# Kernel tuning notes

Measured on AMD Instinct MI355X. Metric: run time of the kernel, lower is better.

The kernel has to match this reference:

```python
import jax, jax.numpy as jnp
import numpy as np

EPS = 1e-5

def _bn(x, g, b):
    # training-mode BatchNorm3d over (N, T, H, W) per channel (axis=1), biased variance
    red = (0, 2, 3, 4)
    m = x.mean(red, keepdims=True)
    v = x.var(red, keepdims=True)
    s = (1, -1, 1, 1, 1)
    return (x - m) / jnp.sqrt(v + EPS) * g.reshape(s) + b.reshape(s)

def _conv3d(x, w, b):
    # Conv3d kernel (1,3,3), padding (0,1,1)
    y = jax.lax.conv_general_dilated(x, w, (1, 1, 1), ((0, 0), (1, 1), (1, 1)),
                                     dimension_numbers=('NCDHW', 'OIDHW', 'NCDHW'))
    return y + b[None, :, None, None, None]

def _forward(x1, x2, attn_weight, W_up, b_up, W_mlp, b_mlp, g_mlp, be_mlp,
             W_c1, b_c1, g_c1, be_c1, W_c2, b_c2, g_c2, be_c2):
    w2 = W_up[:, :, 0]  # [Cin, Cout, 2, 2]
    y = jnp.einsum('bcthw,cokl->bothkwl', x1, w2)
    b_, o, t, h, k, w_, l = y.shape
    x1u = y.reshape(b_, o, t, h * k, w_ * l) + b_up[None, :, None, None, None]

    bs, d_in, T, H, W = x2.shape
    nH = attn_weight.shape[0]
    hh, ww = attn_weight.shape[2], attn_weight.shape[3]
    # [nH, bs, h, w, T, T] -> [nH*bs, T*T, h, w], bilinear upsample to (H, W)
    A = attn_weight.transpose(0, 1, 4, 5, 2, 3).reshape(nH * bs, T * T, hh, ww)
    A = jax.image.resize(A, (nH * bs, T * T, H, W), method='linear')
    A = A.reshape(nH, bs, T, T, H, W)
    # per-(head,b,H,W) temporal attention matmul: avoids materializing x2.repeat(n_head,...)
    ctx = jnp.einsum('nbtsxy,bcsxy->btxycn', A, x2)  # [bs,T,H,W,d_in,nH]
    ctx = ctx.reshape(bs, T, H, W, d_in * nH)        # flatten order (c, n) matches torch permute+view
    hmlp = jnp.einsum('btxyk,ko->btxyo', ctx, W_mlp) + b_mlp
    hmlp = hmlp.transpose(0, 4, 1, 2, 3)  # [bs, enc, T, H, W]
    hmlp = jax.nn.relu(_bn(hmlp, g_mlp, be_mlp))

    x = jnp.concatenate([hmlp, x1u], axis=1)  # [bs, enc+dec, T, H, W]
    x = jax.nn.relu(_bn(_conv3d(x, W_c1, b_c1), g_c1, be_c1))
    x = jax.nn.relu(_bn(_conv3d(x, W_c2, b_c2), g_c2, be_c2))
    return x

def setup_inputs() -> dict:
    key = jax.random.key(0)
    ks = jax.random.split(key, 8)
    bs, T, H, W = 2, 8, 128, 128
    dec, enc, nH = 64, 32, 4
    hh = ww = 16  # attn_scale_factor = 8
    return {
        'x1': jax.random.normal(ks[0], (bs, dec, T, H // 2, W // 2), jnp.float32),
        'x2': jax.random.normal(ks[1], (bs, enc, T, H, W), jnp.float32),
        'attn_weight': jax.random.uniform(ks[2], (nH, bs, hh, ww, T, T), jnp.float32),
        'W_up': jax.random.normal(ks[3], (dec, dec, 1, 2, 2), jnp.float32) * 0.05,
        'b_up': jnp.zeros((dec,), jnp.float32),
        'W_mlp': jax.random.normal(ks[4], (nH * enc, enc), jnp.float32) * 0.05,
        'b_mlp': jnp.zeros((enc,), jnp.float32),
        'g_mlp': jnp.ones((enc,), jnp.float32),
        'be_mlp': jnp.zeros((enc,), jnp.float32),
        'W_c1': jax.random.normal(ks[5], (enc, dec + enc, 1, 3, 3), jnp.float32) * 0.05,
        'b_c1': jnp.zeros((enc,), jnp.float32),
        'g_c1': jnp.ones((enc,), jnp.float32),
        'be_c1': jnp.zeros((enc,), jnp.float32),
        'W_c2': jax.random.normal(ks[6], (enc, enc, 1, 3, 3), jnp.float32) * 0.05,
        'b_c2': jnp.zeros((enc,), jnp.float32),
        'g_c2': jnp.ones((enc,), jnp.float32),
        'be_c2': jnp.zeros((enc,), jnp.float32),
    }

def reference(x1, x2, attn_weight, W_up, b_up, W_mlp, b_mlp, g_mlp, be_mlp,
              W_c1, b_c1, g_c1, be_c1, W_c2, b_c2, g_c2, be_c2):
    return _forward(x1, x2, attn_weight, W_up, b_up, W_mlp, b_mlp, g_mlp, be_mlp,
                    W_c1, b_c1, g_c1, be_c1, W_c2, b_c2, g_c2, be_c2)
```

## Files before the change

kernel.cpp:

```cpp
#include <hip/hip_runtime.h>


#define EPSV 1e-5f

typedef __attribute__((ext_vector_type(8))) short short8;
typedef __attribute__((ext_vector_type(4))) short short4v;
typedef __attribute__((ext_vector_type(4))) float floatx4;

__device__ inline short f2bf(float f) {
  union { float f; unsigned u; } v; v.f = f;
  unsigned r = (v.u + 0x7fffu + ((v.u >> 16) & 1u)) >> 16;
  return (short)r;
}
__device__ inline float bf2f(short s) {
  union { unsigned u; float f; } v; v.u = ((unsigned)(unsigned short)s) << 16;
  return v.f;
}

#define UB_OFF   0
#define HMB_OFF  8388608
#define C1B_OFF  12582912
#define C2B_OFF  16777216
#define X2T_OFF  20971520
#define WB1_OFF  29360128
#define WB2_OFF  29373952
#define WUP_OFF  29378560
#define WMB_OFF  29386752
#define ST_OFF   29388800
#define SC_OFF   29388992

__global__ __launch_bounds__(256) void k_repackb(const float* __restrict__ Wc1, const float* __restrict__ Wc2,
        const float* __restrict__ Wup, const float* __restrict__ Wmlp,
        short* __restrict__ wb1, short* __restrict__ wb2, short* __restrict__ wupb, short* __restrict__ wmb) {
  int i = blockIdx.x*256 + threadIdx.x;
  if (i < 27648) {
    int cc = i / 9216, r = i % 9216;
    int tap = r / 1024, r2 = r % 1024;
    int nt = r2 >> 9, lane = (r2 >> 3) & 63, j = r2 & 7;
    int o = nt*16 + (lane & 15);
    int cin = cc*32 + (lane >> 4)*8 + j;
    wb1[i] = f2bf(Wc1[(o*96 + cin)*9 + tap]);
  }
  if (i < 9216) {
    int tap = i / 1024, r2 = i % 1024;
    int nt = r2 >> 9, lane = (r2 >> 3) & 63, j = r2 & 7;
    int o = nt*16 + (lane & 15);
    int cin = (lane >> 4)*8 + j;
    wb2[i] = f2bf(Wc2[(o*32 + cin)*9 + tap]);
  }
  if (i < 16384) {
    int j = i & 7, lane = (i >> 3) & 63, r = i >> 9;
    int nt = r & 3, kb = (r >> 2) & 1, p = r >> 3;
    int c = kb*32 + (lane >> 4)*8 + j;
    int o = nt*16 + (lane & 15);
    wupb[i] = f2bf(Wup[(c*64 + o)*4 + p]);
  }
  if (i < 4096) {
    int j = i & 7, lane = (i >> 3) & 63, nt = (i >> 9) & 1, ck = i >> 10;
    int k = ck*32 + (lane >> 4)*8 + j;
    int o = nt*16 + (lane & 15);
    wmb[i] = f2bf(Wmlp[k*32 + o]);
  }
}

__global__ __launch_bounds__(256) void k_x2t(const float* __restrict__ x2, short* __restrict__ x2t) {
  __shared__ short lds[32*264];
  int s = blockIdx.y, b = blockIdx.z;
  int tile = blockIdx.x;
  int tid = threadIdx.x;
  #pragma unroll
  for (int k=0; k<8; ++k) {
    int f4 = k*256 + tid;
    int c = f4 >> 6, p4 = f4 & 63;
    float4 v = *(const float4*)(x2 + ((long)(b*32+c)*8 + s)*16384 + tile*256 + p4*4);
    short4v o;
    o[0]=f2bf(v.x); o[1]=f2bf(v.y); o[2]=f2bf(v.z); o[3]=f2bf(v.w);
    *(short4v*)(lds + c*264 + p4*4) = o;
  }
  __syncthreads();
  short* dst = x2t + (((long)(b*8+s)*16384) + tile*256 + tid)*32;
  #pragma unroll
  for (int g=0; g<4; ++g) {
    short8 v;
    #pragma unroll
    for (int j=0; j<8; ++j) v[j] = lds[(g*8+j)*264 + tid];
    *(short8*)(dst + g*8) = v;
  }
}

__global__ __launch_bounds__(256) void k_up_mfma(const float* __restrict__ x1,
        const short* __restrict__ wupb, const float* __restrict__ bup,
        short* __restrict__ Ub) {
  __shared__ __align__(16) char smem[34816];
  short8* stage = (short8*)smem;
  int t = blockIdx.y, b = blockIdx.z;
  int chunk = blockIdx.x >> 2, parity = blockIdx.x & 3;
  int tid = threadIdx.x, lane = tid & 63, w = tid >> 6;

  {
    const float* xp = x1 + ((long)(b*64)*8 + t)*4096 + chunk*256 + tid;
    #pragma unroll
    for (int o8 = 0; o8 < 8; ++o8) {
      short8 v;
      #pragma unroll
      for (int j = 0; j < 8; ++j) v[j] = f2bf(xp[(long)(o8*8+j)*32768]);
      int kb = o8 >> 2, cq = o8 & 3;
      stage[(kb*16 + (tid>>4))*64 + cq*16 + (tid&15)] = v;
    }
  }
  __syncthreads();

  floatx4 acc[4][4];
  #pragma unroll
  for (int nt=0; nt<4; ++nt) {
    float bb = bup[nt*16 + (lane&15)];
    #pragma unroll
    for (int mt=0; mt<4; ++mt) acc[mt][nt] = (floatx4){bb,bb,bb,bb};
  }
  const short8* wp = (const short8*)wupb;
  #pragma unroll
  for (int kb=0; kb<2; ++kb) {
    short8 bfr[4];
    #pragma unroll
    for (int nt=0; nt<4; ++nt) bfr[nt] = wp[((parity*2+kb)*4+nt)*64 + lane];
    #pragma unroll
    for (int mt=0; mt<4; ++mt) {
      short8 a = stage[(kb*16 + w*4 + mt)*64 + lane];
      #pragma unroll
      for (int nt=0; nt<4; ++nt)
        acc[mt][nt] = __builtin_amdgcn_mfma_f32_16x16x32_bf16(a, bfr[nt], acc[mt][nt], 0,0,0);
    }
  }

  __syncthreads();
  short* trb = (short*)smem;
  #pragma unroll
  for (int mt=0; mt<4; ++mt)
    #pragma unroll
    for (int nt=0; nt<4; ++nt)
      #pragma unroll
      for (int r=0; r<4; ++r)
        trb[(w*64 + mt*16 + (lane>>4)*4 + r)*68 + nt*16 + (lane&15)] = f2bf(acc[mt][nt][r]);
  __syncthreads();

  int ip = chunk*256 + tid;
  int X = 2*(ip>>6) + (parity>>1), Y = 2*(ip&63) + (parity&1);
  short* dst = Ub + (((long)(b*8+t)*16384 + X*128 + Y)*64);
  const short* src = trb + tid*68;
  #pragma unroll
  for (int k=0; k<16; ++k)
    *(short4v*)(dst + k*4) = *(const short4v*)(src + k*4);
}

__global__ __launch_bounds__(256) void k_ctxmlp(const short* __restrict__ x2t,
        const float* __restrict__ attn, const short* __restrict__ wmb,
        const float* __restrict__ bmlp, short* __restrict__ HMb, float* __restrict__ st) {
  __shared__ float la[2048];
  __shared__ __align__(16) short ctxs[256*40];
  __shared__ float sb[64];
  int t = blockIdx.y, b = blockIdx.z;
  int tid = threadIdx.x, lane = tid & 63, w = tid >> 6;
  int m = lane & 15, kg = lane >> 4;
  int pos = blockIdx.x*256 + tid;
  if (tid < 64) sb[tid] = 0.f;

  int x0 = blockIdx.x*2;
  int ixbase = max((int)floorf((x0+0.5f)*0.125f - 0.5f), 0);

  float4* la4 = (float4*)la;
  const float4* g4 = (const float4*)attn;
  #pragma unroll
  for (int k=0;k<2;++k) {
    int f = k*256 + tid;
    int s4 = f & 1, iy = (f>>1)&15, slot = (f>>5)&3, n = f>>7;
    int ixs = min(ixbase + slot, 15);
    la4[f] = g4[((((n*2+b)*16+ixs)*16+iy)*8+t)*2 + s4];
  }
  __syncthreads();

  int x = pos >> 7, y = pos & 127;
  float ux = (x+0.5f)*0.125f - 0.5f;
  float uy = (y+0.5f)*0.125f - 0.5f;
  int ix0 = (int)floorf(ux), iy0 = (int)floorf(uy);
  float fx = ux - (float)ix0, fy = uy - (float)iy0;
  int sa  = max(ix0,0) - ixbase;
  int sbl = min(ix0+1,15) - ixbase;
  int iya = max(iy0,0), iyb = min(iy0+1,15);
  float w00=(1.f-fx)*(1.f-fy), w01=(1.f-fx)*fy, w10=fx*(1.f-fy), w11=fx*fy;
  float a[4][8];
  #pragma unroll
  for (int n=0;n<4;++n) {
    const float4* p00 = la4 + ((n*4+sa )*16+iya)*2;
    const float4* p01 = la4 + ((n*4+sa )*16+iyb)*2;
    const float4* p10 = la4 + ((n*4+sbl)*16+iya)*2;
    const float4* p11 = la4 + ((n*4+sbl)*16+iyb)*2;
    #pragma unroll
    for (int q=0;q<2;++q) {
      float4 c00=p00[q], c01=p01[q], c10=p10[q], c11=p11[q];
      a[n][q*4+0] = w00*c00.x + w01*c01.x + w10*c10.x + w11*c11.x;
      a[n][q*4+1] = w00*c00.y + w01*c01.y + w10*c10.y + w11*c11.y;
      a[n][q*4+2] = w00*c00.z + w01*c01.z + w10*c10.z + w11*c11.z;
      a[n][q*4+3] = w00*c00.w + w01*c01.w + w10*c10.w + w11*c11.w;
    }
  }

  float b0v = bmlp[m], b1v = bmlp[16+m];
  floatx4 acc[4][2];
  #pragma unroll
  for (int mt=0; mt<4; ++mt) {
    acc[mt][0] = (floatx4){b0v,b0v,b0v,b0v};
    acc[mt][1] = (floatx4){b1v,b1v,b1v,b1v};
  }

  const short8* wm = (const short8*)wmb;
  for (int ck=0; ck<4; ++ck) {
    short8 xr[8];
    #pragma unroll
    for (int s=0;s<8;++s)
      xr[s] = *(const short8*)(x2t + (((long)(b*8+s)*16384) + pos)*32 + ck*8);
    float ctx[8][4];
    #pragma unroll
    for (int c=0;c<8;++c) { ctx[c][0]=0.f; ctx[c][1]=0.f; ctx[c][2]=0.f; ctx[c][3]=0.f; }
    #pragma unroll
    for (int s=0;s<8;++s) {
      float xv[8];
      #pragma unroll
      for (int c=0;c<8;++c) xv[c] = bf2f(xr[s][c]);
      #pragma unroll
      for (int n=0;n<4;++n) {
        float an = a[n][s];
        #pragma unroll
        for (int c=0;c<8;++c) ctx[c][n] = fmaf(an, xv[c], ctx[c][n]);
      }
    }
    #pragma unroll
    for (int g=0; g<4; ++g) {
      short8 v;
      #pragma unroll
      for (int j=0;j<8;++j) { int kl = g*8+j; v[j] = f2bf(ctx[kl>>2][kl&3]); }
      *(short8*)(ctxs + tid*40 + g*8) = v;
    }
    __syncthreads();
    short8 wb0 = wm[(ck*2+0)*64 + lane];
    short8 wb1f = wm[(ck*2+1)*64 + lane];
    #pragma unroll
    for (int mt=0; mt<4; ++mt) {
      short8 af = *(const short8*)(ctxs + ((w*4+mt)*16 + m)*40 + kg*8);
      acc[mt][0] = __builtin_amdgcn_mfma_f32_16x16x32_bf16(af, wb0,  acc[mt][0], 0,0,0);
      acc[mt][1] = __builtin_amdgcn_mfma_f32_16x16x32_bf16(af, wb1f, acc[mt][1], 0,0,0);
    }
    __syncthreads();
  }

  float s0=0.f,q0=0.f,s1=0.f,q1=0.f;
  #pragma unroll
  for (int mt=0; mt<4; ++mt)
    #pragma unroll
    for (int r=0; r<4; ++r) {
      float v0 = acc[mt][0][r]; s0 += v0; q0 += v0*v0;
      float v1 = acc[mt][1][r]; s1 += v1; q1 += v1*v1;
    }
  s0 += __shfl_xor(s0,16); s0 += __shfl_xor(s0,32);
  q0 += __shfl_xor(q0,16); q0 += __shfl_xor(q0,32);
  s1 += __shfl_xor(s1,16); s1 += __shfl_xor(s1,32);
  q1 += __shfl_xor(q1,16); q1 += __shfl_xor(q1,32);
  if (lane < 16) {
    atomicAdd(&sb[lane],    s0); atomicAdd(&sb[16+lane], s1);
    atomicAdd(&sb[32+lane], q0); atomicAdd(&sb[48+lane], q1);
  }

  short* tr = ctxs;
  #pragma unroll
  for (int mt=0; mt<4; ++mt) {
    int tile = w*4 + mt;
    #pragma unroll
    for (int nt=0; nt<2; ++nt)
      #pragma unroll
      for (int r=0; r<4; ++r)
        tr[(tile*16 + kg*4 + r)*32 + nt*16 + m] = f2bf(acc[mt][nt][r]);
  }
  __syncthreads();
  long slab = (long)(b*8+t)*16384;
  short8* d8 = (short8*)(HMb + (slab + blockIdx.x*256 + tid)*32);
  const short8* s8 = (const short8*)(tr + tid*32);
  d8[0]=s8[0]; d8[1]=s8[1]; d8[2]=s8[2]; d8[3]=s8[3];
  if (tid < 64) atomicAdd(&st[tid], sb[tid]);
}

__global__ void k_finalize(const float* __restrict__ st, const float* __restrict__ g,
                           const float* __restrict__ be, float* __restrict__ sc, float* __restrict__ sh) {
  int c = threadIdx.x;
  if (c < 32) {
    float mean = st[c] * (1.f/262144.f);
    float var  = st[32+c] * (1.f/262144.f) - mean*mean;
    float s = g[c] / sqrtf(var + EPSV);
    sc[c] = s;
    sh[c] = be[c] - mean*s;
  }
}

template<int NCHUNK>
__global__ __launch_bounds__(256) void k_convp(
    const short* __restrict__ src0, const short* __restrict__ srcU,
    const short* __restrict__ wb, const float* __restrict__ bias,
    const float* __restrict__ sc, const float* __restrict__ sh,
    short* __restrict__ dstCL, float* __restrict__ st) {
  constexpr int NBUF = (NCHUNK > 1) ? 2 : 1;
  __shared__ __align__(16) short stage[NBUF][324*40];
  __shared__ float sbuf[64];
  int t = blockIdx.y, b = blockIdx.z;
  int tid = threadIdx.x, lane = tid & 63, w = tid >> 6;
  if (tid < 64) sbuf[tid] = 0.f;
  long slab = (long)(b*8+t)*16384;
  int x0 = (int)(blockIdx.x >> 3) * 16, y0 = (int)(blockIdx.x & 7) * 16;
  int m = lane & 15, kg = lane >> 4;

  int pA = tid;        int rA = pA/18, cA = pA - rA*18;
  int XA = x0-1+rA, YA = y0-1+cA;
  bool okA = ((unsigned)XA < 128u) & ((unsigned)YA < 128u);
  int pB = tid + 256;  bool hasB = pB < 324;
  int rB = pB/18, cB = pB - rB*18;
  int XB = x0-1+rB, YB = y0-1+cB;
  bool okB = hasB && (((unsigned)XB < 128u) & ((unsigned)YB < 128u));
  long offA = slab + XA*128 + YA, offB = slab + XB*128 + YB;

  short8 preA[4], preB[4];

  float bias0 = bias[m], bias1 = bias[16 + m];
  floatx4 acc[4][2];
  #pragma unroll
  for (int mt=0; mt<4; ++mt) {
    acc[mt][0] = (floatx4){bias0,bias0,bias0,bias0};
    acc[mt][1] = (floatx4){bias1,bias1,bias1,bias1};
  }

  {
    const short* sA = src0 + offA*32;
    const short* sB = src0 + offB*32;
    #pragma unroll
    for (int g=0; g<4; ++g) {
      preA[g] = okA ? *(const short8*)(sA + g*8) : (short8)0;
      preB[g] = okB ? *(const short8*)(sB + g*8) : (short8)0;
    }
  }
  #pragma unroll
  for (int g=0; g<4; ++g) {
    short8 vA, vB;
    #pragma unroll
    for (int j=0;j<8;++j) {
      int ch = g*8+j;
      float scv = sc[ch], shv = sh[ch];
      vA[j] = okA ? f2bf(fmaxf(fmaf(bf2f(preA[g][j]), scv, shv), 0.f)) : (short)0;
      vB[j] = okB ? f2bf(fmaxf(fmaf(bf2f(preB[g][j]), scv, shv), 0.f)) : (short)0;
    }
    *(short8*)(&stage[0][pA*40 + g*8]) = vA;
    if (hasB) *(short8*)(&stage[0][pB*40 + g*8]) = vB;
  }
  __syncthreads();

  const short8* wbp = (const short8*)wb;
  #pragma unroll
  for (int cc=0; cc<NCHUNK; ++cc) {
    if (cc+1 < NCHUNK) {
      int coff = cc*32;
      const short* sA = srcU + offA*64 + coff;
      const short* sB = srcU + offB*64 + coff;
      #pragma unroll
      for (int g=0; g<4; ++g) {
        preA[g] = okA ? *(const short8*)(sA + g*8) : (short8)0;
        preB[g] = okB ? *(const short8*)(sB + g*8) : (short8)0;
      }
    }
    #pragma unroll
    for (int tap=0; tap<9; ++tap) {
      int dy = tap/3, dx = tap - 3*dy;
      short8 b0 = wbp[((cc*9+tap)*2+0)*64 + lane];
      short8 b1 = wbp[((cc*9+tap)*2+1)*64 + lane];
      #pragma unroll
      for (int mt=0; mt<4; ++mt) {
        int p = (w*4 + mt + dy)*18 + m + dx;
        short8 a = *(const short8*)(&stage[cc & (NBUF-1)][p*40 + kg*8]);
        acc[mt][0] = __builtin_amdgcn_mfma_f32_16x16x32_bf16(a, b0, acc[mt][0], 0,0,0);
        acc[mt][1] = __builtin_amdgcn_mfma_f32_16x16x32_bf16(a, b1, acc[mt][1], 0,0,0);
      }
    }
    if (cc+1 < NCHUNK) {
      #pragma unroll
      for (int g=0; g<4; ++g) {
        *(short8*)(&stage[(cc+1) & (NBUF-1)][pA*40 + g*8]) = preA[g];
        if (hasB) *(short8*)(&stage[(cc+1) & (NBUF-1)][pB*40 + g*8]) = preB[g];
      }
    }
    __syncthreads();
  }

  float s0=0.f,q0=0.f,s1=0.f,q1=0.f;
  #pragma unroll
  for (int mt=0; mt<4; ++mt)
    #pragma unroll
    for (int r=0; r<4; ++r) {
      float v0 = acc[mt][0][r]; s0 += v0; q0 += v0*v0;
      float v1 = acc[mt][1][r]; s1 += v1; q1 += v1*v1;
    }
  s0 += __shfl_xor(s0,16); s0 += __shfl_xor(s0,32);
  q0 += __shfl_xor(q0,16); q0 += __shfl_xor(q0,32);
  s1 += __shfl_xor(s1,16); s1 += __shfl_xor(s1,32);
  q1 += __shfl_xor(q1,16); q1 += __shfl_xor(q1,32);
  if (lane < 16) {
    atomicAdd(&sbuf[lane],    s0); atomicAdd(&sbuf[16+lane], s1);
    atomicAdd(&sbuf[32+lane], q0); atomicAdd(&sbuf[48+lane], q1);
  }

  short* tr = &stage[0][0];
  #pragma unroll
  for (int mt=0; mt<4; ++mt) {
    int tile = w*4 + mt;
    #pragma unroll
    for (int nt=0; nt<2; ++nt)
      #pragma unroll
      for (int r=0; r<4; ++r)
        tr[(tile*16 + kg*4 + r)*32 + nt*16 + m] = f2bf(acc[mt][nt][r]);
  }
  __syncthreads();
  int px = tid >> 4, py = tid & 15;
  short8* d8 = (short8*)(dstCL + ((slab + (long)(x0+px)*128 + (y0+py))*32));
  const short8* s8 = (const short8*)(tr + tid*32);
  d8[0]=s8[0]; d8[1]=s8[1]; d8[2]=s8[2]; d8[3]=s8[3];
  if (tid < 64) atomicAdd(&st[tid], sbuf[tid]);
}

__global__ __launch_bounds__(256) void k_bnrelu2(const short* __restrict__ C2b,
        const float* __restrict__ sc, const float* __restrict__ sh,
        float* __restrict__ out) {
  __shared__ float tb[10592];
  int t = blockIdx.y, b = blockIdx.z;
  int posbase = blockIdx.x * 256;
  int tid = threadIdx.x;
  long slab = (long)(b*8+t)*16384;
  {
    const short8* sp = (const short8*)(C2b + (slab + posbase + tid)*32);
    int pi = tid + (tid>>5)*8;
    #pragma unroll
    for (int g=0; g<4; ++g) {
      short8 v = sp[g];
      #pragma unroll
      for (int j=0; j<8; ++j) {
        int ch = g*8+j;
        tb[ch*321 + pi] = fmaxf(fmaf(bf2f(v[j]), sc[ch], sh[ch]), 0.f);
      }
    }
  }
  __syncthreads();
  int ch = tid >> 3, pg = tid & 7;
  float* op = out + ((long)(b*32+ch)*8 + t)*16384 + posbase + pg*32;
  const float* tp = tb + ch*321 + pg*40;
  #pragma unroll
  for (int k=0; k<8; ++k) {
    float4 v;
    v.x = tp[k*4+0]; v.y = tp[k*4+1]; v.z = tp[k*4+2]; v.w = tp[k*4+3];
    *(float4*)(op + k*4) = v;
  }
}

extern "C" void kernel_launch(void* const* d_in, const int* in_sizes, int n_in,
                              void* d_out, int out_size, void* d_ws, size_t ws_size,
                              hipStream_t stream) {
  (void)in_sizes; (void)n_in; (void)out_size; (void)ws_size;
  const float* x1   = (const float*)d_in[0];
  const float* x2   = (const float*)d_in[1];
  const float* attn = (const float*)d_in[2];
  const float* Wup  = (const float*)d_in[3];
  const float* bup  = (const float*)d_in[4];
  const float* Wmlp = (const float*)d_in[5];
  const float* bmlp = (const float*)d_in[6];
  const float* gmlp = (const float*)d_in[7];
  const float* bemlp= (const float*)d_in[8];
  const float* Wc1  = (const float*)d_in[9];
  const float* bc1  = (const float*)d_in[10];
  const float* gc1  = (const float*)d_in[11];
  const float* bec1 = (const float*)d_in[12];
  const float* Wc2  = (const float*)d_in[13];
  const float* bc2  = (const float*)d_in[14];
  const float* gc2  = (const float*)d_in[15];
  const float* bec2 = (const float*)d_in[16];
  float* ws  = (float*)d_ws;
  float* out = (float*)d_out;

  short* Ub   = (short*)(ws + UB_OFF);
  short* HMb  = (short*)(ws + HMB_OFF);
  short* C1b  = (short*)(ws + C1B_OFF);
  short* C2b  = (short*)(ws + C2B_OFF);
  short* x2t  = (short*)(ws + X2T_OFF);
  short* wb1  = (short*)(ws + WB1_OFF);
  short* wb2  = (short*)(ws + WB2_OFF);
  short* wupb = (short*)(ws + WUP_OFF);
  short* wmb  = (short*)(ws + WMB_OFF);
  float* st1  = ws + ST_OFF;
  float* st2  = st1 + 64;
  float* st3  = st2 + 64;
  float* sc1  = ws + SC_OFF;  float* sh1 = sc1+32;
  float* sc2  = sh1+32;       float* sh2 = sc2+32;
  float* sc3  = sh2+32;       float* sh3 = sc3+32;

  hipMemsetAsync(st1, 0, 192*sizeof(float), stream);
  k_repackb<<<108, 256, 0, stream>>>(Wc1, Wc2, Wup, Wmlp, wb1, wb2, wupb, wmb);
  k_x2t<<<dim3(64,8,2), 256, 0, stream>>>(x2, x2t);
  k_up_mfma<<<dim3(64,8,2), 256, 0, stream>>>(x1, wupb, bup, Ub);
  k_ctxmlp<<<dim3(64,8,2), 256, 0, stream>>>(x2t, attn, wmb, bmlp, HMb, st1);
  k_finalize<<<1, 32, 0, stream>>>(st1, gmlp, bemlp, sc1, sh1);
  k_convp<3><<<dim3(64,8,2), 256, 0, stream>>>(HMb, Ub, wb1, bc1, sc1, sh1, C1b, st2);
  k_finalize<<<1, 32, 0, stream>>>(st2, gc1, bec1, sc2, sh2);
  k_convp<1><<<dim3(64,8,2), 256, 0, stream>>>(C1b, nullptr, wb2, bc2, sc2, sh2, C2b, st3);
  k_finalize<<<1, 32, 0, stream>>>(st3, gc2, bec2, sc3, sh3);
  k_bnrelu2<<<dim3(64,8,2), 256, 0, stream>>>(C2b, sc3, sh3, out);
}
```

Measured before the change: 308.0 us.

## Drop x2 transpose and finalize kernels; fuse BN stat finalize into consumers

Removes the k_x2t pass so k_ctxmlp reads fp32 x2 directly in channel-first layout. This saves a full read-convert-write pass over x2 but gives up the bf16 vectorised loads. It also removes the three single-block k_finalize launches by computing BN scale and shift per block in shared memory inside the conv and bnrelu kernels. The conv kernel now uses a single stage buffer with an extra barrier between chunks, and hoists the weight fragments for all nine taps into registers before each chunk. That adds register pressure and a serialising sync in exchange for half the LDS.

```diff
diff --git a/kernel.cpp b/kernel.cpp
--- a/kernel.cpp
+++ b/kernel.cpp
@@ -21,13 +21,11 @@
 #define HMB_OFF  8388608
 #define C1B_OFF  12582912
 #define C2B_OFF  16777216
-#define X2T_OFF  20971520
-#define WB1_OFF  29360128
-#define WB2_OFF  29373952
-#define WUP_OFF  29378560
-#define WMB_OFF  29386752
-#define ST_OFF   29388800
-#define SC_OFF   29388992
+#define WB1_OFF  20971520
+#define WB2_OFF  20985344
+#define WUP_OFF  20989952
+#define WMB_OFF  20998144
+#define ST_OFF   21000192
 
 __global__ __launch_bounds__(256) void k_repackb(const float* __restrict__ Wc1, const float* __restrict__ Wc2,
         const float* __restrict__ Wup, const float* __restrict__ Wmlp,
@@ -63,40 +61,16 @@
   }
 }
 
-__global__ __launch_bounds__(256) void k_x2t(const float* __restrict__ x2, short* __restrict__ x2t) {
-  __shared__ short lds[32*264];
-  int s = blockIdx.y, b = blockIdx.z;
-  int tile = blockIdx.x;
-  int tid = threadIdx.x;
-  #pragma unroll
-  for (int k=0; k<8; ++k) {
-    int f4 = k*256 + tid;
-    int c = f4 >> 6, p4 = f4 & 63;
-    float4 v = *(const float4*)(x2 + ((long)(b*32+c)*8 + s)*16384 + tile*256 + p4*4);
-    short4v o;
-    o[0]=f2bf(v.x); o[1]=f2bf(v.y); o[2]=f2bf(v.z); o[3]=f2bf(v.w);
-    *(short4v*)(lds + c*264 + p4*4) = o;
-  }
-  __syncthreads();
-  short* dst = x2t + (((long)(b*8+s)*16384) + tile*256 + tid)*32;
-  #pragma unroll
-  for (int g=0; g<4; ++g) {
-    short8 v;
-    #pragma unroll
-    for (int j=0; j<8; ++j) v[j] = lds[(g*8+j)*264 + tid];
-    *(short8*)(dst + g*8) = v;
-  }
-}
-
-__global__ __launch_bounds__(256) void k_up_mfma(const float* __restrict__ x1,
+__global__ __launch_bounds__(256) void k_up(const float* __restrict__ x1,
         const short* __restrict__ wupb, const float* __restrict__ bup,
         short* __restrict__ Ub) {
   __shared__ __align__(16) char smem[34816];
+  int bid = blockIdx.x;
+  int tid = threadIdx.x;
+  int cp = bid & 63, t = (bid >> 6) & 7, b = bid >> 9;
+  int chunk = cp >> 2, parity = cp & 3;
+  int lane = tid & 63, w = tid >> 6;
   short8* stage = (short8*)smem;
-  int t = blockIdx.y, b = blockIdx.z;
-  int chunk = blockIdx.x >> 2, parity = blockIdx.x & 3;
-  int tid = threadIdx.x, lane = tid & 63, w = tid >> 6;
-
   {
     const float* xp = x1 + ((long)(b*64)*8 + t)*4096 + chunk*256 + tid;
     #pragma unroll
@@ -152,7 +126,7 @@
     *(short4v*)(dst + k*4) = *(const short4v*)(src + k*4);
 }
 
-__global__ __launch_bounds__(256) void k_ctxmlp(const short* __restrict__ x2t,
+__global__ __launch_bounds__(256) void k_ctxmlp(const float* __restrict__ x2,
         const float* __restrict__ attn, const short* __restrict__ wmb,
         const float* __restrict__ bmlp, short* __restrict__ HMb, float* __restrict__ st) {
   __shared__ float la[2048];
@@ -213,24 +187,21 @@
   }
 
   const short8* wm = (const short8*)wmb;
+  const float* x2p = x2 + (long)b*4194304 + pos;
   for (int ck=0; ck<4; ++ck) {
-    short8 xr[8];
-    #pragma unroll
-    for (int s=0;s<8;++s)
-      xr[s] = *(const short8*)(x2t + (((long)(b*8+s)*16384) + pos)*32 + ck*8);
     float ctx[8][4];
     #pragma unroll
     for (int c=0;c<8;++c) { ctx[c][0]=0.f; ctx[c][1]=0.f; ctx[c][2]=0.f; ctx[c][3]=0.f; }
     #pragma unroll
     for (int s=0;s<8;++s) {
-      float xv[8];
-      #pragma unroll
-      for (int c=0;c<8;++c) xv[c] = bf2f(xr[s][c]);
-      #pragma unroll
-      for (int n=0;n<4;++n) {
-        float an = a[n][s];
-        #pragma unroll
-        for (int c=0;c<8;++c) ctx[c][n] = fmaf(an, xv[c], ctx[c][n]);
+      float a0=a[0][s], a1=a[1][s], a2=a[2][s], a3=a[3][s];
+      #pragma unroll
+      for (int c=0;c<8;++c) {
+        float xv = x2p[(long)((ck*8+c)*8 + s)*16384];
+        ctx[c][0] = fmaf(a0, xv, ctx[c][0]);
+        ctx[c][1] = fmaf(a1, xv, ctx[c][1]);
+        ctx[c][2] = fmaf(a2, xv, ctx[c][2]);
+        ctx[c][3] = fmaf(a3, xv, ctx[c][3]);
       }
     }
     #pragma unroll
@@ -287,30 +258,26 @@
   if (tid < 64) atomicAdd(&st[tid], sb[tid]);
 }
 
-__global__ void k_finalize(const float* __restrict__ st, const float* __restrict__ g,
-                           const float* __restrict__ be, float* __restrict__ sc, float* __restrict__ sh) {
-  int c = threadIdx.x;
-  if (c < 32) {
-    float mean = st[c] * (1.f/262144.f);
-    float var  = st[32+c] * (1.f/262144.f) - mean*mean;
-    float s = g[c] / sqrtf(var + EPSV);
-    sc[c] = s;
-    sh[c] = be[c] - mean*s;
-  }
-}
-
 template<int NCHUNK>
 __global__ __launch_bounds__(256) void k_convp(
     const short* __restrict__ src0, const short* __restrict__ srcU,
     const short* __restrict__ wb, const float* __restrict__ bias,
-    const float* __restrict__ sc, const float* __restrict__ sh,
-    short* __restrict__ dstCL, float* __restrict__ st) {
-  constexpr int NBUF = (NCHUNK > 1) ? 2 : 1;
-  __shared__ __align__(16) short stage[NBUF][324*40];
+    const float* __restrict__ stIn, const float* __restrict__ gam,
+    const float* __restrict__ bet,
+    short* __restrict__ dstCL, float* __restrict__ stOut) {
+  __shared__ __align__(16) short stage[324*40];
   __shared__ float sbuf[64];
+  __shared__ float scs[32], shs[32];
   int t = blockIdx.y, b = blockIdx.z;
   int tid = threadIdx.x, lane = tid & 63, w = tid >> 6;
   if (tid < 64) sbuf[tid] = 0.f;
+  if (tid < 32) {
+    float mean = stIn[tid] * (1.f/262144.f);
+    float var  = stIn[32+tid] * (1.f/262144.f) - mean*mean;
+    float s = gam[tid] / sqrtf(var + EPSV);
+    scs[tid] = s;
+    shs[tid] = bet[tid] - mean*s;
+  }
   long slab = (long)(b*8+t)*16384;
   int x0 = (int)(blockIdx.x >> 3) * 16, y0 = (int)(blockIdx.x & 7) * 16;
   int m = lane & 15, kg = lane >> 4;
@@ -343,24 +310,31 @@
       preB[g] = okB ? *(const short8*)(sB + g*8) : (short8)0;
     }
   }
+  __syncthreads();
   #pragma unroll
   for (int g=0; g<4; ++g) {
     short8 vA, vB;
     #pragma unroll
     for (int j=0;j<8;++j) {
       int ch = g*8+j;
-      float scv = sc[ch], shv = sh[ch];
+      float scv = scs[ch], shv = shs[ch];
       vA[j] = okA ? f2bf(fmaxf(fmaf(bf2f(preA[g][j]), scv, shv), 0.f)) : (short)0;
       vB[j] = okB ? f2bf(fmaxf(fmaf(bf2f(preB[g][j]), scv, shv), 0.f)) : (short)0;
     }
-    *(short8*)(&stage[0][pA*40 + g*8]) = vA;
-    if (hasB) *(short8*)(&stage[0][pB*40 + g*8]) = vB;
+    *(short8*)(&stage[pA*40 + g*8]) = vA;
+    if (hasB) *(short8*)(&stage[pB*40 + g*8]) = vB;
   }
   __syncthreads();
 
   const short8* wbp = (const short8*)wb;
   #pragma unroll
   for (int cc=0; cc<NCHUNK; ++cc) {
+    short8 Bf0[9], Bf1[9];
+    #pragma unroll
+    for (int tap=0; tap<9; ++tap) {
+      Bf0[tap] = wbp[((cc*9+tap)*2+0)*64 + lane];
+      Bf1[tap] = wbp[((cc*9+tap)*2+1)*64 + lane];
+    }
     if (cc+1 < NCHUNK) {
       int coff = cc*32;
       const short* sA = srcU + offA*64 + coff;
@@ -374,24 +348,23 @@
     #pragma unroll
     for (int tap=0; tap<9; ++tap) {
       int dy = tap/3, dx = tap - 3*dy;
-      short8 b0 = wbp[((cc*9+tap)*2+0)*64 + lane];
-      short8 b1 = wbp[((cc*9+tap)*2+1)*64 + lane];
       #pragma unroll
       for (int mt=0; mt<4; ++mt) {
         int p = (w*4 + mt + dy)*18 + m + dx;
-        short8 a = *(const short8*)(&stage[cc & (NBUF-1)][p*40 + kg*8]);
-        acc[mt][0] = __builtin_amdgcn_mfma_f32_16x16x32_bf16(a, b0, acc[mt][0], 0,0,0);
-        acc[mt][1] = __builtin_amdgcn_mfma_f32_16x16x32_bf16(a, b1, acc[mt][1], 0,0,0);
+        short8 a = *(const short8*)(&stage[p*40 + kg*8]);
+        acc[mt][0] = __builtin_amdgcn_mfma_f32_16x16x32_bf16(a, Bf0[tap], acc[mt][0], 0,0,0);
+        acc[mt][1] = __builtin_amdgcn_mfma_f32_16x16x32_bf16(a, Bf1[tap], acc[mt][1], 0,0,0);
       }
     }
     if (cc+1 < NCHUNK) {
+      __syncthreads();
       #pragma unroll
       for (int g=0; g<4; ++g) {
-        *(short8*)(&stage[(cc+1) & (NBUF-1)][pA*40 + g*8]) = preA[g];
-        if (hasB) *(short8*)(&stage[(cc+1) & (NBUF-1)][pB*40 + g*8]) = preB[g];
+        *(short8*)(&stage[pA*40 + g*8]) = preA[g];
+        if (hasB) *(short8*)(&stage[pB*40 + g*8]) = preB[g];
       }
-    }
-    __syncthreads();
+      __syncthreads();
+    }
   }
 
   float s0=0.f,q0=0.f,s1=0.f,q1=0.f;
@@ -411,7 +384,8 @@
     atomicAdd(&sbuf[32+lane], q0); atomicAdd(&sbuf[48+lane], q1);
   }
 
-  short* tr = &stage[0][0];
+  __syncthreads();
+  short* tr = &stage[0];
   #pragma unroll
   for (int mt=0; mt<4; ++mt) {
     int tile = w*4 + mt;
@@ -426,27 +400,38 @@
   short8* d8 = (short8*)(dstCL + ((slab + (long)(x0+px)*128 + (y0+py))*32));
   const short8* s8 = (const short8*)(tr + tid*32);
   d8[0]=s8[0]; d8[1]=s8[1]; d8[2]=s8[2]; d8[3]=s8[3];
-  if (tid < 64) atomicAdd(&st[tid], sbuf[tid]);
+  if (tid < 64) atomicAdd(&stOut[tid], sbuf[tid]);
 }
 
 __global__ __launch_bounds__(256) void k_bnrelu2(const short* __restrict__ C2b,
-        const float* __restrict__ sc, const float* __restrict__ sh,
-        float* __restrict__ out) {
+        const float* __restrict__ stIn, const float* __restrict__ gam,
+        const float* __restrict__ bet, float* __restrict__ out) {
   __shared__ float tb[10592];
+  __shared__ float scs[32], shs[32];
   int t = blockIdx.y, b = blockIdx.z;
   int posbase = blockIdx.x * 256;
   int tid = threadIdx.x;
+  if (tid < 32) {
+    float mean = stIn[tid] * (1.f/262144.f);
+    float var  = stIn[32+tid] * (1.f/262144.f) - mean*mean;
+    float s = gam[tid] / sqrtf(var + EPSV);
+    scs[tid] = s;
+    shs[tid] = bet[tid] - mean*s;
+  }
   long slab = (long)(b*8+t)*16384;
+  const short8* sp = (const short8*)(C2b + (slab + posbase + tid)*32);
+  short8 v[4];
+  #pragma unroll
+  for (int g=0; g<4; ++g) v[g] = sp[g];
+  __syncthreads();
   {
-    const short8* sp = (const short8*)(C2b + (slab + posbase + tid)*32);
     int pi = tid + (tid>>5)*8;
     #pragma unroll
     for (int g=0; g<4; ++g) {
-      short8 v = sp[g];
       #pragma unroll
       for (int j=0; j<8; ++j) {
         int ch = g*8+j;
-        tb[ch*321 + pi] = fmaxf(fmaf(bf2f(v[j]), sc[ch], sh[ch]), 0.f);
+        tb[ch*321 + pi] = fmaxf(fmaf(bf2f(v[g][j]), scs[ch], shs[ch]), 0.f);
       }
     }
   }
@@ -456,9 +441,9 @@
   const float* tp = tb + ch*321 + pg*40;
   #pragma unroll
   for (int k=0; k<8; ++k) {
-    float4 v;
-    v.x = tp[k*4+0]; v.y = tp[k*4+1]; v.z = tp[k*4+2]; v.w = tp[k*4+3];
-    *(float4*)(op + k*4) = v;
+    float4 vv;
+    vv.x = tp[k*4+0]; vv.y = tp[k*4+1]; vv.z = tp[k*4+2]; vv.w = tp[k*4+3];
+    *(float4*)(op + k*4) = vv;
   }
 }
 
@@ -490,7 +475,6 @@
   short* HMb  = (short*)(ws + HMB_OFF);
   short* C1b  = (short*)(ws + C1B_OFF);
   short* C2b  = (short*)(ws + C2B_OFF);
-  short* x2t  = (short*)(ws + X2T_OFF);
   short* wb1  = (short*)(ws + WB1_OFF);
   short* wb2  = (short*)(ws + WB2_OFF);
   short* wupb = (short*)(ws + WUP_OFF);
@@ -498,19 +482,12 @@
   float* st1  = ws + ST_OFF;
   float* st2  = st1 + 64;
   float* st3  = st2 + 64;
-  float* sc1  = ws + SC_OFF;  float* sh1 = sc1+32;
-  float* sc2  = sh1+32;       float* sh2 = sc2+32;
-  float* sc3  = sh2+32;       float* sh3 = sc3+32;
 
   hipMemsetAsync(st1, 0, 192*sizeof(float), stream);
   k_repackb<<<108, 256, 0, stream>>>(Wc1, Wc2, Wup, Wmlp, wb1, wb2, wupb, wmb);
-  k_x2t<<<dim3(64,8,2), 256, 0, stream>>>(x2, x2t);
-  k_up_mfma<<<dim3(64,8,2), 256, 0, stream>>>(x1, wupb, bup, Ub);
-  k_ctxmlp<<<dim3(64,8,2), 256, 0, stream>>>(x2t, attn, wmb, bmlp, HMb, st1);
-  k_finalize<<<1, 32, 0, stream>>>(st1, gmlp, bemlp, sc1, sh1);
-  k_convp<3><<<dim3(64,8,2), 256, 0, stream>>>(HMb, Ub, wb1, bc1, sc1, sh1, C1b, st2);
-  k_finalize<<<1, 32, 0, stream>>>(st2, gc1, bec1, sc2, sh2);
-  k_convp<1><<<dim3(64,8,2), 256, 0, stream>>>(C1b, nullptr, wb2, bc2, sc2, sh2, C2b, st3);
-  k_finalize<<<1, 32, 0, stream>>>(st3, gc2, bec2, sc3, sh3);
-  k_bnrelu2<<<dim3(64,8,2), 256, 0, stream>>>(C2b, sc3, sh3, out);
-}
+  k_up<<<1024, 256, 0, stream>>>(x1, wupb, bup, Ub);
+  k_ctxmlp<<<dim3(64,8,2), 256, 0, stream>>>(x2, attn, wmb, bmlp, HMb, st1);
+  k_convp<3><<<dim3(64,8,2), 256, 0, stream>>>(HMb, Ub, wb1, bc1, st1, gmlp, bemlp, C1b, st2);
+  k_convp<1><<<dim3(64,8,2), 256, 0, stream>>>(C1b, nullptr, wb2, bc2, st2, gc1, bec1, C2b, st3);
+  k_bnrelu2<<<dim3(64,8,2), 256, 0, stream>>>(C2b, st3, gc2, bec2, out);
+}
```

After: 312.1 us. Within noise of the previous version (+1.3%).
